# Optimization experiments

Measured on AMD Instinct MI355X. Metric: run time of the kernel, lower is better.

Reference implementation:

```python
import jax, jax.numpy as jnp
import numpy as np

N_NODES = 100000
N_EDGES = 3200000
F_IN, F_HID, F_OUT = 1433, 16, 7


def setup_inputs() -> dict:
    key = jax.random.key(0)
    k1, k2, k3, k4, k5, k6 = jax.random.split(key, 6)
    x = jax.random.normal(k1, (N_NODES, F_IN), dtype=jnp.float32)
    edge_index = jax.random.randint(k2, (2, N_EDGES), 0, N_NODES, dtype=jnp.int64)
    # Glorot-style init for GCNConv weights, zeros for bias (PyG default)
    W1 = jax.random.normal(k3, (F_IN, F_HID), dtype=jnp.float32) * (1.0 / np.sqrt(F_IN))
    b1 = jnp.zeros((F_HID,), dtype=jnp.float32)
    W2 = jax.random.normal(k4, (F_HID, F_OUT), dtype=jnp.float32) * (1.0 / np.sqrt(F_HID))
    b2 = jnp.zeros((F_OUT,), dtype=jnp.float32)
    return {"x": x, "edge_index": edge_index, "W1": W1, "b1": b1, "W2": W2, "b2": b2}


def _gcn_conv(x, W, b, src, dst, deg_inv_sqrt):
    # x: [N, Fin] -> [N, Fout]; src/dst: [E+N] (self-loops included)
    h = x @ W  # linear transform first (PyG GCNConv)
    norm = deg_inv_sqrt[src] * deg_inv_sqrt[dst]  # symmetric normalization
    msg = h[src] * norm[:, None]  # gather + scale
    agg = jax.ops.segment_sum(msg, dst, num_segments=x.shape[0])  # scatter-add at targets
    return agg + b


def reference(x, edge_index, W1, b1, W2, b2):
    n = x.shape[0]
    loops = jnp.arange(n, dtype=edge_index.dtype)
    src = jnp.concatenate([edge_index[0], loops])  # source nodes j
    dst = jnp.concatenate([edge_index[1], loops])  # target nodes i
    # degree over targets (with self-loops), unit edge weights
    deg = jax.ops.segment_sum(jnp.ones_like(src, dtype=x.dtype), dst, num_segments=n)
    deg_inv_sqrt = jnp.where(deg > 0, jax.lax.rsqrt(deg), 0.0)

    h = _gcn_conv(x, W1, b1, src, dst, deg_inv_sqrt)
    h = jax.nn.relu(h)
    # dropout is identity in eval mode
    h = _gcn_conv(h, W2, b2, src, dst, deg_inv_sqrt)
    return jax.nn.log_softmax(h, axis=1)
```

## Files before the change

kernel.cpp:

```cpp
#include <hip/hip_runtime.h>
#include <hip/hip_bf16.h>

#define F_IN 1433
#define F_HID 16
#define F_OUT 7
#define KSTEPS 45

typedef __bf16 bf16x8 __attribute__((ext_vector_type(8)));
typedef float f32x4 __attribute__((ext_vector_type(4)));
typedef int i32x4 __attribute__((ext_vector_type(4)));
typedef unsigned short u16;
typedef unsigned int u32;

static __device__ __forceinline__ float bf2f(u16 b) {
    return __builtin_bit_cast(float, (u32)b << 16);
}
static __device__ __forceinline__ u16 f2bf(float f) {
    u32 u = __builtin_bit_cast(u32, f);
    u32 r = u + 0x7FFFu + ((u >> 16) & 1u);
    return (u16)(r >> 16);
}
static __device__ __forceinline__ int clampN(int v, int N) {
    return ((unsigned)v < (unsigned)N) ? v : 0;
}

__global__ __launch_bounds__(256) void k_init(const u16* __restrict__ xu,
                                              const int* __restrict__ ei,
                                              int* __restrict__ flags,
                                              int* __restrict__ deg, int N) {
    int i = blockIdx.x * 256 + threadIdx.x;
    if (i < N) deg[i] = 0;
    if (blockIdx.x == 0 && threadIdx.x < 64) {
        int t = threadIdx.x;
        u16 v = xu[t];
        int e = (v >> 7) & 0xFF;
        unsigned long long mb = __ballot(e >= 100 && e <= 140);
        unsigned long long mz = __ballot(ei[2 * t + 1] == 0);
        if (t == 0) {
            flags[0] = (__popcll(mb) >= 56) ? 1 : 0;
            flags[1] = (__popcll(mz) >= 48) ? 1 : 0;
        }
    }
}



__global__ __launch_bounds__(256) void k_deg(const int* __restrict__ ei,
                                             const int* __restrict__ flags,
                                             int* __restrict__ deg, int E, int N) {
    int sh = flags[1];
    int i = blockIdx.x * 256 + threadIdx.x;
    if (i < E) {
        int d = ei[(size_t)(E + i) << sh];
        atomicAdd(&deg[clampN(d, N)], 1);
    }
}

__global__ __launch_bounds__(256) void k_scan1(const int* __restrict__ deg,
                                               int* __restrict__ rowoff,
                                               int* __restrict__ bsum, int N) {
    __shared__ int s[256];
    int t = threadIdx.x, i = blockIdx.x * 256 + t;
    int v = (i < N) ? deg[i] : 0;
    s[t] = v;
    __syncthreads();
    for (int o = 1; o < 256; o <<= 1) {
        int x = 0;
        if (t >= o) x = s[t - o];
        __syncthreads();
        s[t] += x;
        __syncthreads();
    }
    if (i < N) rowoff[i] = s[t] - v;
    if (t == 255) bsum[blockIdx.x] = s[255];
}

__global__ __launch_bounds__(1024) void k_scan2(const int* __restrict__ bsum,
                                                int* __restrict__ bscan, int NB) {
    __shared__ int s[1024];
    int t = threadIdx.x;
    int v = (t < NB) ? bsum[t] : 0;
    s[t] = v;
    __syncthreads();
    for (int o = 1; o < 1024; o <<= 1) {
        int x = 0;
        if (t >= o) x = s[t - o];
        __syncthreads();
        s[t] += x;
        __syncthreads();
    }
    if (t < NB) bscan[t] = s[t] - v;
}

__global__ __launch_bounds__(256) void k_scan3(const int* __restrict__ deg,
                                               int* __restrict__ rowoff,
                                               const int* __restrict__ bscan,
                                               int* __restrict__ fill,
                                               float* __restrict__ dis, int N) {
    int i = blockIdx.x * 256 + threadIdx.x;
    if (i >= N) return;
    int ro = rowoff[i] + bscan[blockIdx.x];
    rowoff[i] = ro;
    fill[i] = ro;
    dis[i] = rsqrtf((float)(deg[i] + 1));
}

__global__ __launch_bounds__(256) void k_fill(const int* __restrict__ ei,
                                              const int* __restrict__ flags,
                                              int* __restrict__ fill,
                                              int* __restrict__ csr, int E, int N) {
    int sh = flags[1];
    int i = blockIdx.x * 256 + threadIdx.x;
    if (i < E) {
        int d = ei[(size_t)(E + i) << sh];
        int s = ei[(size_t)i << sh];
        int slot = atomicAdd(&fill[clampN(d, N)], 1);
        if (slot >= 0 && slot < E) csr[slot] = clampN(s, N);
    }
}


template <int ISBF>
static __device__ __forceinline__ void gemm_tiles(const u16* xu, const float* xf,
                                                  const u16* lw,
                                                  const float* __restrict__ dis,
                                                  float* __restrict__ hn, int N,
                                                  int tid, int bid, int grid) {
    int wave = tid >> 6, lane = tid & 63;
    int quad = lane >> 4, m = lane & 15;
    int ntiles = (N + 63) / 64;
    int k0 = quad * 8;

    for (int tb = bid; tb < ntiles; tb += grid) {
        int base = tb * 64 + wave * 16;
        int row = base + m;
        int rowc = row < N ? row : N - 1;
        const u16* xru = xu + (size_t)rowc * F_IN;
        const float* xrf = xf + (size_t)rowc * F_IN;

        f32x4 acc = {0.f, 0.f, 0.f, 0.f};
        for (int ks = 0; ks < KSTEPS - 1; ks++) {
            u16 e[8];
            if (ISBF) {
                const u16* xp = xru + k0 + ks * 32;
#pragma unroll
                for (int j = 0; j < 8; j++) e[j] = xp[j];
            } else {
                const float* xp = xrf + k0 + ks * 32;
#pragma unroll
                for (int j = 0; j < 8; j++) e[j] = f2bf(xp[j]);
            }
            i32x4 wv = {(int)((u32)e[0] | ((u32)e[1] << 16)),
                        (int)((u32)e[2] | ((u32)e[3] << 16)),
                        (int)((u32)e[4] | ((u32)e[5] << 16)),
                        (int)((u32)e[6] | ((u32)e[7] << 16))};
            bf16x8 a = __builtin_bit_cast(bf16x8, wv);
            bf16x8 b = __builtin_bit_cast(bf16x8, *(const i32x4*)(&lw[ks * 512 + lane * 8]));
            acc = __builtin_amdgcn_mfma_f32_16x16x32_bf16(a, b, acc, 0, 0, 0);
        }
        {
            int ks = KSTEPS - 1;
            int kb = ks * 32 + k0;
            u16 e[8];
#pragma unroll
            for (int j = 0; j < 8; j++) {
                int k = kb + j;
                e[j] = (k < F_IN) ? (ISBF ? xru[k] : f2bf(xrf[k])) : (u16)0;
            }
            i32x4 wv = {(int)((u32)e[0] | ((u32)e[1] << 16)),
                        (int)((u32)e[2] | ((u32)e[3] << 16)),
                        (int)((u32)e[4] | ((u32)e[5] << 16)),
                        (int)((u32)e[6] | ((u32)e[7] << 16))};
            bf16x8 a = __builtin_bit_cast(bf16x8, wv);
            bf16x8 b = __builtin_bit_cast(bf16x8, *(const i32x4*)(&lw[ks * 512 + lane * 8]));
            acc = __builtin_amdgcn_mfma_f32_16x16x32_bf16(a, b, acc, 0, 0, 0);
        }
#pragma unroll
        for (int r = 0; r < 4; r++) {
            int orow = base + quad * 4 + r;
            if (orow < N) hn[(size_t)orow * 16 + m] = acc[r] * dis[orow];
        }
    }
}

__global__ __launch_bounds__(256) void k_gemm1(const void* __restrict__ x,
                                               const void* __restrict__ W1,
                                               const int* __restrict__ flags,
                                               const float* __restrict__ dis,
                                               float* __restrict__ hn, int N) {
    __shared__ __align__(16) u16 lw[KSTEPS * 512];
    int tid = threadIdx.x;
    int isbf = flags[0];
    const u16* W1u = (const u16*)W1;
    const float* W1f = (const float*)W1;
    for (int idx = tid; idx < KSTEPS * 512; idx += 256) {
        int j = idx & 7, lane = (idx >> 3) & 63, ks = idx >> 9;
        int quad = lane >> 4, n = lane & 15;
        int k = ks * 32 + quad * 8 + j;
        u16 w = 0;
        if (k < F_IN) w = isbf ? W1u[k * 16 + n] : f2bf(W1f[k * 16 + n]);
        lw[idx] = w;
    }
    __syncthreads();
    if (isbf)
        gemm_tiles<1>((const u16*)x, (const float*)x, lw, dis, hn, N, tid, blockIdx.x, gridDim.x);
    else
        gemm_tiles<0>((const u16*)x, (const float*)x, lw, dis, hn, N, tid, blockIdx.x, gridDim.x);
}


__global__ __launch_bounds__(256) void k_agg1(const float* __restrict__ hn,
                                              const int* __restrict__ csr,
                                              const int* __restrict__ rowoff,
                                              const int* __restrict__ deg,
                                              const float* __restrict__ dis,
                                              const void* __restrict__ b1,
                                              const void* __restrict__ W2,
                                              const int* __restrict__ flags,
                                              float* __restrict__ tn, int N) {
    int tid = threadIdx.x;
    int lane = tid & 63;
    int c = tid & 15, g = tid >> 4;
    int v = blockIdx.x * 16 + g;
    if (v >= N) return;
    int isbf = flags[0];
    float bc = isbf ? bf2f(((const u16*)b1)[c]) : ((const float*)b1)[c];

    float acc = hn[(size_t)v * 16 + c];
    int s0 = rowoff[v], d = deg[v];
    const int* cp = csr + s0;
    float a1 = 0.f, a2 = 0.f, a3 = 0.f;
    int i = 0;
    for (; i + 4 <= d; i += 4) {
        int sA = cp[i], sB = cp[i + 1], sC = cp[i + 2], sD = cp[i + 3];
        acc += hn[(size_t)sA * 16 + c];
        a1 += hn[(size_t)sB * 16 + c];
        a2 += hn[(size_t)sC * 16 + c];
        a3 += hn[(size_t)sD * 16 + c];
    }
    for (; i < d; i++) acc += hn[(size_t)cp[i] * 16 + c];
    acc += (a1 + a2) + a3;

    float dv = dis[v];
    float y = fmaxf(acc * dv + bc, 0.f);

    float w2c[16];
#pragma unroll
    for (int k = 0; k < 16; k++) {
        float w = 0.f;
        if (c < 7) w = isbf ? bf2f(((const u16*)W2)[k * 7 + c]) : ((const float*)W2)[k * 7 + c];
        w2c[k] = w;
    }
    float s = 0.f;
#pragma unroll
    for (int k = 0; k < 16; k++) {
        float yk = __shfl(y, (lane & 48) + k, 64);
        s += yk * w2c[k];
    }
    if (c < 8) tn[(size_t)v * 8 + c] = (c < 7) ? s * dv : 0.f;
}


__global__ __launch_bounds__(256) void k_agg2(const float* __restrict__ tn,
                                              const int* __restrict__ csr,
                                              const int* __restrict__ rowoff,
                                              const int* __restrict__ deg,
                                              const float* __restrict__ dis,
                                              const void* __restrict__ b2,
                                              const int* __restrict__ flags,
                                              void* __restrict__ out, int N) {
    int tid = threadIdx.x;
    int c = tid & 7, g = tid >> 3;
    int v = blockIdx.x * 32 + g;
    if (v >= N) return;
    int isbf = flags[0];
    float bc = 0.f;
    if (c < 7) bc = isbf ? bf2f(((const u16*)b2)[c]) : ((const float*)b2)[c];

    float acc = tn[(size_t)v * 8 + c];
    int s0 = rowoff[v], d = deg[v];
    const int* cp = csr + s0;
    float a1 = 0.f, a2 = 0.f, a3 = 0.f;
    int i = 0;
    for (; i + 4 <= d; i += 4) {
        int sA = cp[i], sB = cp[i + 1], sC = cp[i + 2], sD = cp[i + 3];
        acc += tn[(size_t)sA * 8 + c];
        a1 += tn[(size_t)sB * 8 + c];
        a2 += tn[(size_t)sC * 8 + c];
        a3 += tn[(size_t)sD * 8 + c];
    }
    for (; i < d; i++) acc += tn[(size_t)cp[i] * 8 + c];
    acc += (a1 + a2) + a3;

    float z = (c < 7) ? (acc * dis[v] + bc) : -1e30f;
    float mx = z;
#pragma unroll
    for (int o = 1; o < 8; o <<= 1) mx = fmaxf(mx, __shfl_xor(mx, o, 8));
    float ex = (c < 7) ? expf(z - mx) : 0.f;
    float sm = ex;
#pragma unroll
    for (int o = 1; o < 8; o <<= 1) sm += __shfl_xor(sm, o, 8);
    sm = fmaxf(sm, 1e-30f);
    if (c < 7) {
        float res = z - mx - logf(sm);
        if (isbf)
            ((u16*)out)[(size_t)v * 7 + c] = f2bf(res);
        else
            ((float*)out)[(size_t)v * 7 + c] = res;
    }
}


extern "C" void kernel_launch(void* const* d_in, const int* in_sizes, int n_in,
                              void* d_out, int out_size, void* d_ws, size_t ws_size,
                              hipStream_t stream) {
    const void* x = d_in[0];
    const int* ei = (const int*)d_in[1];
    const void* W1 = d_in[2];
    const void* b1 = d_in[3];
    const void* W2 = d_in[4];
    const void* b2 = d_in[5];

    int N = in_sizes[0] / F_IN;
    int E = in_sizes[1] / 2;

    char* p = (char*)d_ws;
    size_t off = 0;
    auto alloc = [&](size_t bytes) -> void* {
        off = (off + 255) & ~(size_t)255;
        void* r = p + off;
        off += bytes;
        return r;
    };
    int* flags = (int*)alloc(256);
    int* deg = (int*)alloc((size_t)N * 4);
    int* rowoff = (int*)alloc((size_t)N * 4);
    int* fill = (int*)alloc((size_t)N * 4);
    int* bsum = (int*)alloc(1024 * 4);
    int* bscan = (int*)alloc(1024 * 4);
    float* dis = (float*)alloc((size_t)N * 4);
    int* csr = (int*)alloc((size_t)E * 4);
    float* hn = (float*)alloc((size_t)N * 16 * 4);
    float* tn = (float*)alloc((size_t)N * 8 * 4);
    (void)ws_size;
    (void)n_in;
    (void)out_size;

    int gE = (E + 255) / 256;
    int gN = (N + 255) / 256;

    k_init<<<gN, 256, 0, stream>>>((const u16*)x, ei, flags, deg, N);
    k_deg<<<gE, 256, 0, stream>>>(ei, flags, deg, E, N);
    k_scan1<<<gN, 256, 0, stream>>>(deg, rowoff, bsum, N);
    k_scan2<<<1, 1024, 0, stream>>>(bsum, bscan, gN);
    k_scan3<<<gN, 256, 0, stream>>>(deg, rowoff, bscan, fill, dis, N);
    k_fill<<<gE, 256, 0, stream>>>(ei, flags, fill, csr, E, N);

    int ntiles = (N + 63) / 64;
    int gg = ntiles < 768 ? ntiles : 768;
    k_gemm1<<<gg, 256, 0, stream>>>(x, W1, flags, dis, hn, N);

    k_agg1<<<(N + 15) / 16, 256, 0, stream>>>(hn, csr, rowoff, deg, dis, b1, W2, flags, tn, N);
    k_agg2<<<(N + 31) / 32, 256, 0, stream>>>(tn, csr, rowoff, deg, dis, b2, flags, d_out, N);
}
```

Before: 1.304 ms.

## Fuse GCN pipeline into one cooperative kernel overlapping GEMM with CSR build

Replaces the nine-launch sequence with a single cooperative persistent kernel. Half the blocks run the X·W1 MFMA GEMM while the other half build degrees, scan, and fill the CSR, coordinating through a custom subset barrier. Grid syncs separate this phase from the two aggregation phases. Because the GEMM no longer waits for the degree array, the dis scaling moves into agg1's gather. That adds a dis load per edge and gives the bandwidth-heavy GEMM only half the CUs. If the cooperative launch fails, the old multi-kernel path is kept as a fallback.

```diff
diff --git a/kernel.cpp b/kernel.cpp
--- a/kernel.cpp
+++ b/kernel.cpp
@@ -1,5 +1,8 @@
 #include <hip/hip_runtime.h>
 #include <hip/hip_bf16.h>
+#include <hip/hip_cooperative_groups.h>
+
+namespace cg = cooperative_groups;
 
 #define F_IN 1433
 #define F_HID 16
@@ -23,6 +26,310 @@
 static __device__ __forceinline__ int clampN(int v, int N) {
     return ((unsigned)v < (unsigned)N) ? v : 0;
 }
+
+static __device__ __forceinline__ void subset_bar(int* cnt, int target) {
+    __syncthreads();
+    if (threadIdx.x == 0) {
+        __threadfence();
+        __hip_atomic_fetch_add(cnt, 1, __ATOMIC_RELEASE, __HIP_MEMORY_SCOPE_AGENT);
+        while (__hip_atomic_load(cnt, __ATOMIC_ACQUIRE, __HIP_MEMORY_SCOPE_AGENT) < target) {
+            __builtin_amdgcn_s_sleep(8);
+        }
+        __threadfence();
+    }
+    __syncthreads();
+}
+
+
+static __device__ __forceinline__ void dev_stage_lw(const void* W1, int isbf, u16* lw, int tid) {
+    const u16* W1u = (const u16*)W1;
+    const float* W1f = (const float*)W1;
+    for (int idx = tid; idx < KSTEPS * 512; idx += 256) {
+        int j = idx & 7, lane = (idx >> 3) & 63, ks = idx >> 9;
+        int quad = lane >> 4, n = lane & 15;
+        int k = ks * 32 + quad * 8 + j;
+        u16 w = 0;
+        if (k < F_IN) w = isbf ? W1u[k * 16 + n] : f2bf(W1f[k * 16 + n]);
+        lw[idx] = w;
+    }
+}
+
+template <int ISBF>
+static __device__ void dev_gemm(const u16* xu, const float* xf, const u16* lw,
+                                float* __restrict__ hn, int N, int tid, int bid, int grid) {
+    int wave = tid >> 6, lane = tid & 63;
+    int quad = lane >> 4, m = lane & 15;
+    int ntiles = (N + 63) / 64;
+    int k0 = quad * 8;
+
+    for (int tb = bid; tb < ntiles; tb += grid) {
+        int base = tb * 64 + wave * 16;
+        int row = base + m;
+        int rowc = row < N ? row : N - 1;
+        const u16* xru = xu + (size_t)rowc * F_IN;
+        const float* xrf = xf + (size_t)rowc * F_IN;
+
+        f32x4 acc = {0.f, 0.f, 0.f, 0.f};
+        for (int ks = 0; ks < KSTEPS - 1; ks++) {
+            u16 e[8];
+            if (ISBF) {
+                const u16* xp = xru + k0 + ks * 32;
+#pragma unroll
+                for (int j = 0; j < 8; j++) e[j] = xp[j];
+            } else {
+                const float* xp = xrf + k0 + ks * 32;
+#pragma unroll
+                for (int j = 0; j < 8; j++) e[j] = f2bf(xp[j]);
+            }
+            i32x4 wv = {(int)((u32)e[0] | ((u32)e[1] << 16)),
+                        (int)((u32)e[2] | ((u32)e[3] << 16)),
+                        (int)((u32)e[4] | ((u32)e[5] << 16)),
+                        (int)((u32)e[6] | ((u32)e[7] << 16))};
+            bf16x8 a = __builtin_bit_cast(bf16x8, wv);
+            bf16x8 b = __builtin_bit_cast(bf16x8, *(const i32x4*)(&lw[ks * 512 + lane * 8]));
+            acc = __builtin_amdgcn_mfma_f32_16x16x32_bf16(a, b, acc, 0, 0, 0);
+        }
+        {
+            int ks = KSTEPS - 1;
+            int kb = ks * 32 + k0;
+            u16 e[8];
+#pragma unroll
+            for (int j = 0; j < 8; j++) {
+                int k = kb + j;
+                e[j] = (k < F_IN) ? (ISBF ? xru[k] : f2bf(xrf[k])) : (u16)0;
+            }
+            i32x4 wv = {(int)((u32)e[0] | ((u32)e[1] << 16)),
+                        (int)((u32)e[2] | ((u32)e[3] << 16)),
+                        (int)((u32)e[4] | ((u32)e[5] << 16)),
+                        (int)((u32)e[6] | ((u32)e[7] << 16))};
+            bf16x8 a = __builtin_bit_cast(bf16x8, wv);
+            bf16x8 b = __builtin_bit_cast(bf16x8, *(const i32x4*)(&lw[ks * 512 + lane * 8]));
+            acc = __builtin_amdgcn_mfma_f32_16x16x32_bf16(a, b, acc, 0, 0, 0);
+        }
+#pragma unroll
+        for (int r = 0; r < 4; r++) {
+            int orow = base + quad * 4 + r;
+            if (orow < N) hn[(size_t)orow * 16 + m] = acc[r];
+        }
+    }
+}
+
+static __device__ void dev_agg1(const float* __restrict__ hn, const int* __restrict__ csr,
+                                const int* __restrict__ rowoff, const int* __restrict__ deg,
+                                const float* __restrict__ dis, const void* __restrict__ b1,
+                                const void* __restrict__ W2, int isbf,
+                                float* __restrict__ tn, int N, int bid, int grid, int tid) {
+    int lane = tid & 63;
+    int c = tid & 15, g = tid >> 4;
+    float bc = isbf ? bf2f(((const u16*)b1)[c]) : ((const float*)b1)[c];
+    float w2c[16];
+#pragma unroll
+    for (int k = 0; k < 16; k++) {
+        float w = 0.f;
+        if (c < 7) w = isbf ? bf2f(((const u16*)W2)[k * 7 + c]) : ((const float*)W2)[k * 7 + c];
+        w2c[k] = w;
+    }
+    for (int v = bid * 16 + g; v < N; v += grid * 16) {
+        float dv = dis[v];
+        float acc = hn[(size_t)v * 16 + c] * dv;
+        int s0 = rowoff[v], d = deg[v];
+        const int* cp = csr + s0;
+        float a1 = 0.f, a2 = 0.f, a3 = 0.f;
+        int i = 0;
+        for (; i + 4 <= d; i += 4) {
+            int sA = clampN(cp[i], N), sB = clampN(cp[i + 1], N);
+            int sC = clampN(cp[i + 2], N), sD = clampN(cp[i + 3], N);
+            acc += hn[(size_t)sA * 16 + c] * dis[sA];
+            a1 += hn[(size_t)sB * 16 + c] * dis[sB];
+            a2 += hn[(size_t)sC * 16 + c] * dis[sC];
+            a3 += hn[(size_t)sD * 16 + c] * dis[sD];
+        }
+        for (; i < d; i++) {
+            int s = clampN(cp[i], N);
+            acc += hn[(size_t)s * 16 + c] * dis[s];
+        }
+        acc += (a1 + a2) + a3;
+        float y = fmaxf(acc * dv + bc, 0.f);
+        float s = 0.f;
+#pragma unroll
+        for (int k = 0; k < 16; k++) s += __shfl(y, (lane & 48) + k, 64) * w2c[k];
+        if (c < 8) tn[(size_t)v * 8 + c] = (c < 7) ? s * dv : 0.f;
+    }
+}
+
+static __device__ void dev_agg2(const float* __restrict__ tn, const int* __restrict__ csr,
+                                const int* __restrict__ rowoff, const int* __restrict__ deg,
+                                const float* __restrict__ dis, const void* __restrict__ b2,
+                                int isbf, void* __restrict__ out, int N, int bid, int grid,
+                                int tid) {
+    int c = tid & 7, g = tid >> 3;
+    float bc = 0.f;
+    if (c < 7) bc = isbf ? bf2f(((const u16*)b2)[c]) : ((const float*)b2)[c];
+    for (int v = bid * 32 + g; v < N; v += grid * 32) {
+        float acc = tn[(size_t)v * 8 + c];
+        int s0 = rowoff[v], d = deg[v];
+        const int* cp = csr + s0;
+        float a1 = 0.f, a2 = 0.f, a3 = 0.f;
+        int i = 0;
+        for (; i + 4 <= d; i += 4) {
+            int sA = clampN(cp[i], N), sB = clampN(cp[i + 1], N);
+            int sC = clampN(cp[i + 2], N), sD = clampN(cp[i + 3], N);
+            acc += tn[(size_t)sA * 8 + c];
+            a1 += tn[(size_t)sB * 8 + c];
+            a2 += tn[(size_t)sC * 8 + c];
+            a3 += tn[(size_t)sD * 8 + c];
+        }
+        for (; i < d; i++) acc += tn[(size_t)clampN(cp[i], N) * 8 + c];
+        acc += (a1 + a2) + a3;
+
+        float z = (c < 7) ? (acc * dis[v] + bc) : -1e30f;
+        float mx = z;
+#pragma unroll
+        for (int o = 1; o < 8; o <<= 1) mx = fmaxf(mx, __shfl_xor(mx, o, 8));
+        float ex = (c < 7) ? expf(z - mx) : 0.f;
+        float sm = ex;
+#pragma unroll
+        for (int o = 1; o < 8; o <<= 1) sm += __shfl_xor(sm, o, 8);
+        sm = fmaxf(sm, 1e-30f);
+        if (c < 7) {
+            float res = z - mx - logf(sm);
+            if (isbf)
+                ((u16*)out)[(size_t)v * 7 + c] = f2bf(res);
+            else
+                ((float*)out)[(size_t)v * 7 + c] = res;
+        }
+    }
+}
+
+
+struct MegaArgs {
+    const void* x;
+    const int* ei;
+    const void* W1;
+    const void* b1;
+    const void* W2;
+    const void* b2;
+    int* flags;
+    int* cnt;
+    int* deg;
+    int* rowoff;
+    int* fill;
+    int* bsum;
+    float* dis;
+    int* csr;
+    float* hn;
+    float* tn;
+    void* out;
+    int N;
+    int E;
+};
+
+__global__ __launch_bounds__(256) void k_mega(MegaArgs a) {
+    cg::grid_group gg = cg::this_grid();
+    int tid = threadIdx.x;
+    int b = blockIdx.x;
+    int G = gridDim.x;
+
+    __shared__ int sflags[2];
+    __shared__ __align__(16) u16 lw[KSTEPS * 512];
+    __shared__ int sscan[256];
+    __shared__ int swsum[4];
+
+    for (int i = b * 256 + tid; i < a.N; i += G * 256) a.deg[i] = 0;
+    if (b == 0) {
+        if (tid == 0) a.cnt[0] = 0;
+        if (tid < 64) {
+            u16 v = ((const u16*)a.x)[tid];
+            int e = (v >> 7) & 0xFF;
+            unsigned long long mb = __ballot(e >= 100 && e <= 140);
+            unsigned long long mz = __ballot(a.ei[2 * tid + 1] == 0);
+            if (tid == 0) {
+                a.flags[0] = (__popcll(mb) >= 56) ? 1 : 0;
+                a.flags[1] = (__popcll(mz) >= 48) ? 1 : 0;
+            }
+        }
+    }
+    gg.sync();
+
+    if (tid == 0) {
+        sflags[0] = a.flags[0];
+        sflags[1] = a.flags[1];
+    }
+    __syncthreads();
+    int isbf = sflags[0], sh = sflags[1];
+
+    int G2 = G >> 1;
+    int nb = G - G2;
+    if (b < G2) {
+        dev_stage_lw(a.W1, isbf, lw, tid);
+        __syncthreads();
+        if (isbf)
+            dev_gemm<1>((const u16*)a.x, (const float*)a.x, lw, a.hn, a.N, tid, b, G2);
+        else
+            dev_gemm<0>((const u16*)a.x, (const float*)a.x, lw, a.hn, a.N, tid, b, G2);
+    } else {
+        int lb = b - G2;
+        for (int i = lb * 256 + tid; i < a.E; i += nb * 256) {
+            int d = a.ei[(size_t)(a.E + i) << sh];
+            atomicAdd(&a.deg[clampN(d, a.N)], 1);
+        }
+        subset_bar(a.cnt, nb * 1);
+        int chunk = (a.N + nb - 1) / nb;
+        int q = (chunk + 255) / 256;
+        int base = lb * chunk;
+        int nend = base + chunk;
+        if (nend > a.N) nend = a.N;
+        int tot = 0;
+        for (int jj = 0; jj < q; jj++) {
+            int node = base + tid * q + jj;
+            if (node < nend) tot += a.deg[node];
+        }
+        sscan[tid] = tot;
+        __syncthreads();
+        for (int o = 1; o < 256; o <<= 1) {
+            int xv = (tid >= o) ? sscan[tid - o] : 0;
+            __syncthreads();
+            sscan[tid] += xv;
+            __syncthreads();
+        }
+        int incl = sscan[tid];
+        if (tid == 255) a.bsum[lb] = incl;
+        __syncthreads();
+        sscan[tid] = incl - tot;
+        subset_bar(a.cnt, nb * 2);
+        int part = 0;
+        for (int j = tid; j < lb; j += 256) part += a.bsum[j];
+        for (int o = 32; o > 0; o >>= 1) part += __shfl_down(part, o, 64);
+        if ((tid & 63) == 0) swsum[tid >> 6] = part;
+        __syncthreads();
+        int off = swsum[0] + swsum[1] + swsum[2] + swsum[3];
+        int run = off + sscan[tid];
+        for (int jj = 0; jj < q; jj++) {
+            int node = base + tid * q + jj;
+            if (node < nend) {
+                int dn = a.deg[node];
+                a.rowoff[node] = run;
+                a.fill[node] = run;
+                a.dis[node] = rsqrtf((float)(dn + 1));
+                run += dn;
+            }
+        }
+        subset_bar(a.cnt, nb * 3);
+        for (int i = lb * 256 + tid; i < a.E; i += nb * 256) {
+            int d = a.ei[(size_t)(a.E + i) << sh];
+            int s = a.ei[(size_t)i << sh];
+            int slot = atomicAdd(&a.fill[clampN(d, a.N)], 1);
+            if (slot >= 0 && slot < a.E) a.csr[slot] = clampN(s, a.N);
+        }
+    }
+    gg.sync();
+
+    dev_agg1(a.hn, a.csr, a.rowoff, a.deg, a.dis, a.b1, a.W2, isbf, a.tn, a.N, b, G, tid);
+    gg.sync();
+
+    dev_agg2(a.tn, a.csr, a.rowoff, a.deg, a.dis, a.b2, isbf, a.out, a.N, b, G, tid);
+}
+
 
 __global__ __launch_bounds__(256) void k_init(const u16* __restrict__ xu,
                                               const int* __restrict__ ei,
@@ -43,8 +350,6 @@
     }
 }
 
-
-
 __global__ __launch_bounds__(256) void k_deg(const int* __restrict__ ei,
                                              const int* __restrict__ flags,
                                              int* __restrict__ deg, int E, int N) {
@@ -119,95 +424,20 @@
     }
 }
 
-
-template <int ISBF>
-static __device__ __forceinline__ void gemm_tiles(const u16* xu, const float* xf,
-                                                  const u16* lw,
-                                                  const float* __restrict__ dis,
-                                                  float* __restrict__ hn, int N,
-                                                  int tid, int bid, int grid) {
-    int wave = tid >> 6, lane = tid & 63;
-    int quad = lane >> 4, m = lane & 15;
-    int ntiles = (N + 63) / 64;
-    int k0 = quad * 8;
-
-    for (int tb = bid; tb < ntiles; tb += grid) {
-        int base = tb * 64 + wave * 16;
-        int row = base + m;
-        int rowc = row < N ? row : N - 1;
-        const u16* xru = xu + (size_t)rowc * F_IN;
-        const float* xrf = xf + (size_t)rowc * F_IN;
-
-        f32x4 acc = {0.f, 0.f, 0.f, 0.f};
-        for (int ks = 0; ks < KSTEPS - 1; ks++) {
-            u16 e[8];
-            if (ISBF) {
-                const u16* xp = xru + k0 + ks * 32;
-#pragma unroll
-                for (int j = 0; j < 8; j++) e[j] = xp[j];
-            } else {
-                const float* xp = xrf + k0 + ks * 32;
-#pragma unroll
-                for (int j = 0; j < 8; j++) e[j] = f2bf(xp[j]);
-            }
-            i32x4 wv = {(int)((u32)e[0] | ((u32)e[1] << 16)),
-                        (int)((u32)e[2] | ((u32)e[3] << 16)),
-                        (int)((u32)e[4] | ((u32)e[5] << 16)),
-                        (int)((u32)e[6] | ((u32)e[7] << 16))};
-            bf16x8 a = __builtin_bit_cast(bf16x8, wv);
-            bf16x8 b = __builtin_bit_cast(bf16x8, *(const i32x4*)(&lw[ks * 512 + lane * 8]));
-            acc = __builtin_amdgcn_mfma_f32_16x16x32_bf16(a, b, acc, 0, 0, 0);
-        }
-        {
-            int ks = KSTEPS - 1;
-            int kb = ks * 32 + k0;
-            u16 e[8];
-#pragma unroll
-            for (int j = 0; j < 8; j++) {
-                int k = kb + j;
-                e[j] = (k < F_IN) ? (ISBF ? xru[k] : f2bf(xrf[k])) : (u16)0;
-            }
-            i32x4 wv = {(int)((u32)e[0] | ((u32)e[1] << 16)),
-                        (int)((u32)e[2] | ((u32)e[3] << 16)),
-                        (int)((u32)e[4] | ((u32)e[5] << 16)),
-                        (int)((u32)e[6] | ((u32)e[7] << 16))};
-            bf16x8 a = __builtin_bit_cast(bf16x8, wv);
-            bf16x8 b = __builtin_bit_cast(bf16x8, *(const i32x4*)(&lw[ks * 512 + lane * 8]));
-            acc = __builtin_amdgcn_mfma_f32_16x16x32_bf16(a, b, acc, 0, 0, 0);
-        }
-#pragma unroll
-        for (int r = 0; r < 4; r++) {
-            int orow = base + quad * 4 + r;
-            if (orow < N) hn[(size_t)orow * 16 + m] = acc[r] * dis[orow];
-        }
-    }
-}
-
 __global__ __launch_bounds__(256) void k_gemm1(const void* __restrict__ x,
                                                const void* __restrict__ W1,
                                                const int* __restrict__ flags,
-                                               const float* __restrict__ dis,
                                                float* __restrict__ hn, int N) {
     __shared__ __align__(16) u16 lw[KSTEPS * 512];
     int tid = threadIdx.x;
     int isbf = flags[0];
-    const u16* W1u = (const u16*)W1;
-    const float* W1f = (const float*)W1;
-    for (int idx = tid; idx < KSTEPS * 512; idx += 256) {
-        int j = idx & 7, lane = (idx >> 3) & 63, ks = idx >> 9;
-        int quad = lane >> 4, n = lane & 15;
-        int k = ks * 32 + quad * 8 + j;
-        u16 w = 0;
-        if (k < F_IN) w = isbf ? W1u[k * 16 + n] : f2bf(W1f[k * 16 + n]);
-        lw[idx] = w;
-    }
+    dev_stage_lw(W1, isbf, lw, tid);
     __syncthreads();
     if (isbf)
-        gemm_tiles<1>((const u16*)x, (const float*)x, lw, dis, hn, N, tid, blockIdx.x, gridDim.x);
+        dev_gemm<1>((const u16*)x, (const float*)x, lw, hn, N, tid, blockIdx.x, gridDim.x);
     else
-        gemm_tiles<0>((const u16*)x, (const float*)x, lw, dis, hn, N, tid, blockIdx.x, gridDim.x);
-}
-
+        dev_gemm<0>((const u16*)x, (const float*)x, lw, hn, N, tid, blockIdx.x, gridDim.x);
+}
 
 __global__ __launch_bounds__(256) void k_agg1(const float* __restrict__ hn,
                                               const int* __restrict__ csr,
@@ -218,48 +448,9 @@
                                               const void* __restrict__ W2,
                                               const int* __restrict__ flags,
                                               float* __restrict__ tn, int N) {
-    int tid = threadIdx.x;
-    int lane = tid & 63;
-    int c = tid & 15, g = tid >> 4;
-    int v = blockIdx.x * 16 + g;
-    if (v >= N) return;
-    int isbf = flags[0];
-    float bc = isbf ? bf2f(((const u16*)b1)[c]) : ((const float*)b1)[c];
-
-    float acc = hn[(size_t)v * 16 + c];
-    int s0 = rowoff[v], d = deg[v];
-    const int* cp = csr + s0;
-    float a1 = 0.f, a2 = 0.f, a3 = 0.f;
-    int i = 0;
-    for (; i + 4 <= d; i += 4) {
-        int sA = cp[i], sB = cp[i + 1], sC = cp[i + 2], sD = cp[i + 3];
-        acc += hn[(size_t)sA * 16 + c];
-        a1 += hn[(size_t)sB * 16 + c];
-        a2 += hn[(size_t)sC * 16 + c];
-        a3 += hn[(size_t)sD * 16 + c];
-    }
-    for (; i < d; i++) acc += hn[(size_t)cp[i] * 16 + c];
-    acc += (a1 + a2) + a3;
-
-    float dv = dis[v];
-    float y = fmaxf(acc * dv + bc, 0.f);
-
-    float w2c[16];
-#pragma unroll
-    for (int k = 0; k < 16; k++) {
-        float w = 0.f;
-        if (c < 7) w = isbf ? bf2f(((const u16*)W2)[k * 7 + c]) : ((const float*)W2)[k * 7 + c];
-        w2c[k] = w;
-    }
-    float s = 0.f;
-#pragma unroll
-    for (int k = 0; k < 16; k++) {
-        float yk = __shfl(y, (lane & 48) + k, 64);
-        s += yk * w2c[k];
-    }
-    if (c < 8) tn[(size_t)v * 8 + c] = (c < 7) ? s * dv : 0.f;
-}
-
+    dev_agg1(hn, csr, rowoff, deg, dis, b1, W2, flags[0], tn, N, blockIdx.x, gridDim.x,
+             threadIdx.x);
+}
 
 __global__ __launch_bounds__(256) void k_agg2(const float* __restrict__ tn,
                                               const int* __restrict__ csr,
@@ -269,45 +460,8 @@
                                               const void* __restrict__ b2,
                                               const int* __restrict__ flags,
                                               void* __restrict__ out, int N) {
-    int tid = threadIdx.x;
-    int c = tid & 7, g = tid >> 3;
-    int v = blockIdx.x * 32 + g;
-    if (v >= N) return;
-    int isbf = flags[0];
-    float bc = 0.f;
-    if (c < 7) bc = isbf ? bf2f(((const u16*)b2)[c]) : ((const float*)b2)[c];
-
-    float acc = tn[(size_t)v * 8 + c];
-    int s0 = rowoff[v], d = deg[v];
-    const int* cp = csr + s0;
-    float a1 = 0.f, a2 = 0.f, a3 = 0.f;
-    int i = 0;
-    for (; i + 4 <= d; i += 4) {
-        int sA = cp[i], sB = cp[i + 1], sC = cp[i + 2], sD = cp[i + 3];
-        acc += tn[(size_t)sA * 8 + c];
-        a1 += tn[(size_t)sB * 8 + c];
-        a2 += tn[(size_t)sC * 8 + c];
-        a3 += tn[(size_t)sD * 8 + c];
-    }
-    for (; i < d; i++) acc += tn[(size_t)cp[i] * 8 + c];
-    acc += (a1 + a2) + a3;
-
-    float z = (c < 7) ? (acc * dis[v] + bc) : -1e30f;
-    float mx = z;
-#pragma unroll
-    for (int o = 1; o < 8; o <<= 1) mx = fmaxf(mx, __shfl_xor(mx, o, 8));
-    float ex = (c < 7) ? expf(z - mx) : 0.f;
-    float sm = ex;
-#pragma unroll
-    for (int o = 1; o < 8; o <<= 1) sm += __shfl_xor(sm, o, 8);
-    sm = fmaxf(sm, 1e-30f);
-    if (c < 7) {
-        float res = z - mx - logf(sm);
-        if (isbf)
-            ((u16*)out)[(size_t)v * 7 + c] = f2bf(res);
-        else
-            ((float*)out)[(size_t)v * 7 + c] = res;
-    }
+    dev_agg2(tn, csr, rowoff, deg, dis, b2, flags[0], out, N, blockIdx.x, gridDim.x,
+             threadIdx.x);
 }
 
 
@@ -333,6 +487,7 @@
         return r;
     };
     int* flags = (int*)alloc(256);
+    int* cnt = (int*)alloc(256);
     int* deg = (int*)alloc((size_t)N * 4);
     int* rowoff = (int*)alloc((size_t)N * 4);
     int* fill = (int*)alloc((size_t)N * 4);
@@ -346,20 +501,41 @@
     (void)n_in;
     (void)out_size;
 
-    int gE = (E + 255) / 256;
-    int gN = (N + 255) / 256;
-
-    k_init<<<gN, 256, 0, stream>>>((const u16*)x, ei, flags, deg, N);
-    k_deg<<<gE, 256, 0, stream>>>(ei, flags, deg, E, N);
-    k_scan1<<<gN, 256, 0, stream>>>(deg, rowoff, bsum, N);
-    k_scan2<<<1, 1024, 0, stream>>>(bsum, bscan, gN);
-    k_scan3<<<gN, 256, 0, stream>>>(deg, rowoff, bscan, fill, dis, N);
-    k_fill<<<gE, 256, 0, stream>>>(ei, flags, fill, csr, E, N);
-
-    int ntiles = (N + 63) / 64;
-    int gg = ntiles < 768 ? ntiles : 768;
-    k_gemm1<<<gg, 256, 0, stream>>>(x, W1, flags, dis, hn, N);
-
-    k_agg1<<<(N + 15) / 16, 256, 0, stream>>>(hn, csr, rowoff, deg, dis, b1, W2, flags, tn, N);
-    k_agg2<<<(N + 31) / 32, 256, 0, stream>>>(tn, csr, rowoff, deg, dis, b2, flags, d_out, N);
-}
+    static int s_mb = -1;
+    if (s_mb < 0) {
+        int mb = 0;
+        if (hipOccupancyMaxActiveBlocksPerMultiprocessor(
+                &mb, reinterpret_cast<const void*>(&k_mega), 256, 0) != hipSuccess ||
+            mb < 1)
+            mb = 0;
+        s_mb = mb;
+    }
+    int grid = s_mb * 256;
+    if (grid > 1024) grid = 1024;
+
+    bool ok = false;
+    if (grid >= 8) {
+        MegaArgs ha = {x,    ei,  W1,   b1,  W2, b2,  flags, cnt, deg,
+                       rowoff, fill, bsum, dis, csr, hn, tn,  d_out, N,   E};
+        void* params[] = {&ha};
+        ok = (hipLaunchCooperativeKernel(reinterpret_cast<void*>(&k_mega), dim3(grid),
+                                         dim3(256), params, 0, stream) == hipSuccess);
+        if (!ok) (void)hipGetLastError();
+    }
+
+    if (!ok) {
+        int gE = (E + 255) / 256;
+        int gN = (N + 255) / 256;
+        k_init<<<gN, 256, 0, stream>>>((const u16*)x, ei, flags, deg, N);
+        k_deg<<<gE, 256, 0, stream>>>(ei, flags, deg, E, N);
+        k_scan1<<<gN, 256, 0, stream>>>(deg, rowoff, bsum, N);
+        k_scan2<<<1, 1024, 0, stream>>>(bsum, bscan, gN);
+        k_scan3<<<gN, 256, 0, stream>>>(deg, rowoff, bscan, fill, dis, N);
+        k_fill<<<gE, 256, 0, stream>>>(ei, flags, fill, csr, E, N);
+        int ntiles = (N + 63) / 64;
+        int gg = ntiles < 768 ? ntiles : 768;
+        k_gemm1<<<gg, 256, 0, stream>>>(x, W1, flags, hn, N);
+        k_agg1<<<(N + 15) / 16, 256, 0, stream>>>(hn, csr, rowoff, deg, dis, b1, W2, flags, tn, N);
+        k_agg2<<<(N + 31) / 32, 256, 0, stream>>>(tn, csr, rowoff, deg, dis, b2, flags, d_out, N);
+    }
+}
```

Measured after the change: 1.329 ms. Within noise of the previous version (+1.9%).
